# Optimization experiments

Measured on AMD Instinct MI355X. Metric: run time of the kernel, lower is better.

Reference implementation:

```python
import jax, jax.numpy as jnp
import numpy as np
import math

D = 1280      # embed_dim ('650M')
H = 20        # n_head
DH = D // H   # d_hidden = 64
DFF = 4 * D   # r_ff = 4
LN_EPS = 1e-5


def layer_norm(x, gamma, beta):
    mu = jnp.mean(x, axis=-1, keepdims=True)
    var = jnp.var(x, axis=-1, keepdims=True)
    return (x - mu) * jax.lax.rsqrt(var + LN_EPS) * gamma + beta


def setup_inputs() -> dict:
    key = jax.random.key(0)
    ks = jax.random.split(key, 16)
    B, L = 2, 2048
    x = jax.random.normal(ks[0], (B, L, D), dtype=jnp.float32)
    y = jax.random.normal(ks[1], (B, L, D), dtype=jnp.float32)  # dm_embeds (unused by module)
    s_qkv = 1.0 / math.sqrt(D)
    Wq = jax.random.uniform(ks[2], (D, D), jnp.float32, -s_qkv, s_qkv)
    Wk = jax.random.uniform(ks[3], (D, D), jnp.float32, -s_qkv, s_qkv)
    Wv = jax.random.uniform(ks[4], (D, D), jnp.float32, -s_qkv, s_qkv)
    Wo = jax.random.uniform(ks[5], (D, D), jnp.float32, -s_qkv, s_qkv)
    bo = jnp.zeros((D,), jnp.float32)
    W1 = jax.random.normal(ks[6], (D, DFF), jnp.float32) * math.sqrt(2.0 / D)  # kaiming
    b1 = jnp.zeros((DFF,), jnp.float32)
    W2 = jax.random.uniform(ks[7], (DFF, D), jnp.float32, -1.0 / math.sqrt(DFF), 1.0 / math.sqrt(DFF))
    b2 = jnp.zeros((D,), jnp.float32)
    g1 = jnp.ones((D,), jnp.float32); be1 = jnp.zeros((D,), jnp.float32)
    g2 = jnp.ones((D,), jnp.float32); be2 = jnp.zeros((D,), jnp.float32)
    return dict(x=x, y=y, Wq=Wq, Wk=Wk, Wv=Wv, Wo=Wo, bo=bo,
                W1=W1, b1=b1, W2=W2, b2=b2, g1=g1, be1=be1, g2=g2, be2=be2)


def reference(x, y, Wq, Wk, Wv, Wo, bo, W1, b1, W2, b2, g1, be1, g2, be2):
    B, L, _ = x.shape
    scaling = 1.0 / math.sqrt(DH)
    # --- pre-norm self-attention ---
    xn = layer_norm(x, g1, be1)
    q = (xn @ Wq).reshape(B, L, H, DH) * scaling
    k = (xn @ Wk).reshape(B, L, H, DH)
    v = (xn @ Wv).reshape(B, L, H, DH)
    scores = jnp.einsum('bqhd,bkhd->bhqk', q, k)
    attn = jax.nn.softmax(scores, axis=-1)
    o = jnp.einsum('bhqk,bkhd->bqhd', attn, v).reshape(B, L, D)
    x = x + (o @ Wo + bo)
    # --- pre-norm FFN ---
    xn = layer_norm(x, g2, be2)
    h = jax.nn.relu(xn @ W1 + b1)
    x = x + (h @ W2 + b2)
    return x
```

## Files before the change

kernel.cpp:

```cpp
#include <hip/hip_runtime.h>

typedef short bf16x8 __attribute__((ext_vector_type(8)));
typedef short bf16x4 __attribute__((ext_vector_type(4)));
typedef float f32x4 __attribute__((ext_vector_type(4)));
typedef unsigned short u16;

#define GL16(g, l) __builtin_amdgcn_global_load_lds( \
    (const __attribute__((address_space(1))) void*)(g), \
    (__attribute__((address_space(3))) void*)(l), 16, 0, 0)

__device__ __forceinline__ u16 f2bf(float f) {
  union { float f; unsigned u; } v; v.f = f;
  return (u16)((v.u + 0x7fffu + ((v.u >> 16) & 1u)) >> 16);
}

__device__ __forceinline__ float exp2_(float x) {
#if __has_builtin(__builtin_amdgcn_exp2f)
  return __builtin_amdgcn_exp2f(x);
#else
  return __expf(x * 0.69314718056f);
#endif
}

__device__ __forceinline__ unsigned cvtpk(float a, float b) {
  unsigned r;
  asm("v_cvt_pk_bf16_f32 %0, %1, %2" : "=v"(r) : "v"(a), "v"(b));
  return r;
}

__global__ __launch_bounds__(256) void ln_kernel(
    const float* __restrict__ x, const float* __restrict__ g,
    const float* __restrict__ b, u16* __restrict__ out) {
  const int row = blockIdx.x, tid = threadIdx.x;
  const float4* xr = (const float4*)(x + (size_t)row * 1280);
  float4 v1 = xr[tid];
  float4 v2 = make_float4(0.f, 0.f, 0.f, 0.f);
  if (tid < 64) v2 = xr[256 + tid];
  float s = v1.x + v1.y + v1.z + v1.w + v2.x + v2.y + v2.z + v2.w;
  float q = v1.x * v1.x + v1.y * v1.y + v1.z * v1.z + v1.w * v1.w +
            v2.x * v2.x + v2.y * v2.y + v2.z * v2.z + v2.w * v2.w;
#pragma unroll
  for (int off = 32; off >= 1; off >>= 1) {
    s += __shfl_xor(s, off);
    q += __shfl_xor(q, off);
  }
  __shared__ float sm[8];
  if ((tid & 63) == 0) { sm[tid >> 6] = s; sm[4 + (tid >> 6)] = q; }
  __syncthreads();
  s = sm[0] + sm[1] + sm[2] + sm[3];
  q = sm[4] + sm[5] + sm[6] + sm[7];
  const float mean = s * (1.0f / 1280.0f);
  const float rstd = rsqrtf(q * (1.0f / 1280.0f) - mean * mean + 1e-5f);
  const float4* gr = (const float4*)g;
  const float4* br = (const float4*)b;
  u16* orow = out + (size_t)row * 1280;
  {
    float4 gg = gr[tid], bb = br[tid];
    ushort4 o;
    o.x = f2bf((v1.x - mean) * rstd * gg.x + bb.x);
    o.y = f2bf((v1.y - mean) * rstd * gg.y + bb.y);
    o.z = f2bf((v1.z - mean) * rstd * gg.z + bb.z);
    o.w = f2bf((v1.w - mean) * rstd * gg.w + bb.w);
    *(ushort4*)&orow[tid * 4] = o;
  }
  if (tid < 64) {
    float4 gg = gr[256 + tid], bb = br[256 + tid];
    ushort4 o;
    o.x = f2bf((v2.x - mean) * rstd * gg.x + bb.x);
    o.y = f2bf((v2.y - mean) * rstd * gg.y + bb.y);
    o.z = f2bf((v2.z - mean) * rstd * gg.z + bb.z);
    o.w = f2bf((v2.w - mean) * rstd * gg.w + bb.w);
    *(ushort4*)&orow[(256 + tid) * 4] = o;
  }
}

__global__ __launch_bounds__(256) void tconv_kernel(
    const float* __restrict__ src, u16* __restrict__ dst,
    int rows, int cols, float scale) {
  __shared__ float t[64][33];
  const int tid = threadIdx.x;
  const size_t c0 = (size_t)blockIdx.x * 64, r0 = (size_t)blockIdx.y * 32;
  const int ty = tid >> 4, col4 = tid & 15;
#pragma unroll
  for (int i = 0; i < 2; ++i) {
    const int row = ty + i * 16;
    float4 v = *(const float4*)&src[(r0 + row) * cols + c0 + col4 * 4];
    t[col4 * 4 + 0][row] = v.x;
    t[col4 * 4 + 1][row] = v.y;
    t[col4 * 4 + 2][row] = v.z;
    t[col4 * 4 + 3][row] = v.w;
  }
  __syncthreads();
  const int c = tid >> 2, rb = (tid & 3) * 8;
  ushort4 o1, o2;
  o1.x = f2bf(t[c][rb + 0] * scale); o1.y = f2bf(t[c][rb + 1] * scale);
  o1.z = f2bf(t[c][rb + 2] * scale); o1.w = f2bf(t[c][rb + 3] * scale);
  o2.x = f2bf(t[c][rb + 4] * scale); o2.y = f2bf(t[c][rb + 5] * scale);
  o2.z = f2bf(t[c][rb + 6] * scale); o2.w = f2bf(t[c][rb + 7] * scale);
  u16* d = &dst[(c0 + c) * rows + r0 + rb];
  *(ushort4*)d = o1;
  *(ushort4*)(d + 4) = o2;
}

__global__ __launch_bounds__(256) void tconv3_kernel(
    const float* __restrict__ s0, const float* __restrict__ s1,
    const float* __restrict__ s2, u16* __restrict__ dst, float scale0) {
  __shared__ float t[64][33];
  const int tid = threadIdx.x, z = blockIdx.z;
  const float* src = (z == 0) ? s0 : ((z == 1) ? s1 : s2);
  const float scale = (z == 0) ? scale0 : 1.0f;
  u16* d0 = dst + (size_t)z * 1280 * 1280;
  const size_t c0 = (size_t)blockIdx.x * 64, r0 = (size_t)blockIdx.y * 32;
  const int ty = tid >> 4, col4 = tid & 15;
#pragma unroll
  for (int i = 0; i < 2; ++i) {
    const int row = ty + i * 16;
    float4 v = *(const float4*)&src[(r0 + row) * 1280 + c0 + col4 * 4];
    t[col4 * 4 + 0][row] = v.x;
    t[col4 * 4 + 1][row] = v.y;
    t[col4 * 4 + 2][row] = v.z;
    t[col4 * 4 + 3][row] = v.w;
  }
  __syncthreads();
  const int c = tid >> 2, rb = (tid & 3) * 8;
  ushort4 o1, o2;
  o1.x = f2bf(t[c][rb + 0] * scale); o1.y = f2bf(t[c][rb + 1] * scale);
  o1.z = f2bf(t[c][rb + 2] * scale); o1.w = f2bf(t[c][rb + 3] * scale);
  o2.x = f2bf(t[c][rb + 4] * scale); o2.y = f2bf(t[c][rb + 5] * scale);
  o2.z = f2bf(t[c][rb + 6] * scale); o2.w = f2bf(t[c][rb + 7] * scale);
  u16* d = &d0[(c0 + c) * 1280 + r0 + rb];
  *(ushort4*)d = o1;
  *(ushort4*)(d + 4) = o2;
}

__global__ __launch_bounds__(256) void vtrans_kernel(const u16* __restrict__ qkv,
                                                     u16* __restrict__ vt) {
  __shared__ u16 t[64][65];
  const int tx = threadIdx.x & 63, ty = threadIdx.x >> 6;
  const int t0 = blockIdx.x * 64, bh = blockIdx.y, b = bh / 20, h = bh % 20;
  const u16* src = qkv + (size_t)b * 2048 * 3840 + 2560 + h * 64;
  for (int i = ty; i < 64; i += 4) t[i][tx] = src[(size_t)(t0 + i) * 3840 + tx];
  __syncthreads();
  u16* dst = vt + (size_t)bh * 64 * 2048 + t0;
  for (int i = ty; i < 64; i += 4) dst[(size_t)i * 2048 + tx] = t[tx][i];
}

__global__ __launch_bounds__(256) void initadd_kernel(
    const float* __restrict__ src, const float* __restrict__ bias,
    float* __restrict__ out) {
  const size_t i = (size_t)blockIdx.x * 256 + threadIdx.x;
  float4 v = ((const float4*)src)[i];
  float4 b = ((const float4*)bias)[i % 320];
  v.x += b.x; v.y += b.y; v.z += b.z; v.w += b.w;
  ((float4*)out)[i] = v;
}

template <int EPI>
__device__ __forceinline__ void gemm_body(
    const u16* __restrict__ A, const u16* __restrict__ BT,
    const float* __restrict__ bias, void* __restrict__ out,
    int M, int N, int K, int kSteps) {
  __shared__ __attribute__((aligned(16))) u16 Als[3][128 * 32];
  __shared__ __attribute__((aligned(16))) u16 Bls[3][128 * 32];
  const int tid = threadIdx.x;
  const int w = tid >> 6, lane = tid & 63;
  const int lo = lane & 15, hi = lane >> 4;
  const int wm = w >> 1, wn = w & 1;
  const int gx = gridDim.x, gxy = gx * gridDim.y;
  const int nwg = gxy * gridDim.z;
  int s = blockIdx.x + gx * blockIdx.y + gxy * blockIdx.z;
  s = (s & 7) * (nwg >> 3) + (s >> 3);
  const int bz = s / gxy; s -= bz * gxy;
  const int by = s / gx;  const int bx = s - by * gx;
  const size_t m0 = (size_t)by * 128, n0 = (size_t)bx * 128;
  const int kt0 = bz * kSteps;
  f32x4 acc[4][4] = {};
  const int srow = w * 32 + (lane >> 2);
  const int scol = ((lane & 3) ^ ((lane >> 3) & 3)) * 8;
  const int rsw = (lo >> 1) & 3;
#define STAGE(buf, kt)                                                        \
  do {                                                                        \
    const size_t kb = (size_t)(kt) * 32 + scol;                               \
    GL16(&A[(m0 + srow) * K + kb],       &Als[buf][(w * 2 + 0) * 512]);       \
    GL16(&A[(m0 + srow + 16) * K + kb],  &Als[buf][(w * 2 + 1) * 512]);       \
    GL16(&BT[(n0 + srow) * K + kb],      &Bls[buf][(w * 2 + 0) * 512]);       \
    GL16(&BT[(n0 + srow + 16) * K + kb], &Bls[buf][(w * 2 + 1) * 512]);       \
  } while (0)
  STAGE(0, kt0 + 0);
  STAGE(1, kt0 + 1);
  int cur = 0;
  for (int t = 0; t < kSteps; ++t) {
    if (t + 1 < kSteps) asm volatile("s_waitcnt vmcnt(4)" ::: "memory");
    else                asm volatile("s_waitcnt vmcnt(0)" ::: "memory");
    __builtin_amdgcn_s_barrier();
    __builtin_amdgcn_sched_barrier(0);
    const int nxt = (cur == 0) ? 2 : cur - 1;
    if (t + 2 < kSteps) STAGE(nxt, kt0 + t + 2);
    bf16x8 af[4], bfr[4];
#pragma unroll
    for (int mi = 0; mi < 4; ++mi)
      af[mi] = *(const bf16x8*)&Als[cur][(wm * 64 + mi * 16 + lo) * 32 + ((hi ^ rsw) * 8)];
#pragma unroll
    for (int ni = 0; ni < 4; ++ni)
      bfr[ni] = *(const bf16x8*)&Bls[cur][(wn * 64 + ni * 16 + lo) * 32 + ((hi ^ rsw) * 8)];
#pragma unroll
    for (int mi = 0; mi < 4; ++mi)
#pragma unroll
      for (int ni = 0; ni < 4; ++ni)
        acc[mi][ni] = __builtin_amdgcn_mfma_f32_16x16x32_bf16(
            af[mi], bfr[ni], acc[mi][ni], 0, 0, 0);
    cur = (cur == 2) ? 0 : cur + 1;
  }
#undef STAGE
#pragma unroll
  for (int ni = 0; ni < 4; ++ni) {
    const size_t col = n0 + wn * 64 + ni * 16 + lo;
    const float bv = (EPI == 1) ? bias[col] : 0.0f;
#pragma unroll
    for (int mi = 0; mi < 4; ++mi) {
      const size_t rb = m0 + wm * 64 + mi * 16 + hi * 4;
#pragma unroll
      for (int r = 0; r < 4; ++r) {
        const size_t idx = (rb + r) * N + col;
        float v = acc[mi][ni][r];
        if (EPI == 0) {
          ((u16*)out)[idx] = f2bf(v);
        } else if (EPI == 1) {
          v += bv;
          v = fmaxf(v, 0.0f);
          ((u16*)out)[idx] = f2bf(v);
        } else {
          atomicAdd(&((float*)out)[idx], v);
        }
      }
    }
  }
}

__global__ __launch_bounds__(256, 3) void gemm_qkv(
    const u16* __restrict__ A, const u16* __restrict__ BT,
    void* __restrict__ out, int M, int N, int K, int kSteps) {
  gemm_body<0>(A, BT, nullptr, out, M, N, K, kSteps);
}
__global__ __launch_bounds__(256, 3) void gemm_oproj(
    const u16* __restrict__ A, const u16* __restrict__ BT,
    void* __restrict__ out, int M, int N, int K, int kSteps) {
  gemm_body<3>(A, BT, nullptr, out, M, N, K, kSteps);
}
__global__ __launch_bounds__(256, 3) void gemm_ffn1(
    const u16* __restrict__ A, const u16* __restrict__ BT,
    const float* __restrict__ bias, void* __restrict__ out,
    int M, int N, int K, int kSteps) {
  gemm_body<1>(A, BT, bias, out, M, N, K, kSteps);
}
__global__ __launch_bounds__(256, 3) void gemm_ffn2(
    const u16* __restrict__ A, const u16* __restrict__ BT,
    void* __restrict__ out, int M, int N, int K, int kSteps) {
  gemm_body<3>(A, BT, nullptr, out, M, N, K, kSteps);
}

__global__ __launch_bounds__(256) void attn_kernel(
    const u16* __restrict__ qkv, const u16* __restrict__ vt,
    u16* __restrict__ aout) {
  __shared__ __attribute__((aligned(16))) u16 Klds[64 * 64];
  __shared__ __attribute__((aligned(16))) u16 Vlds[64 * 64];
  __shared__ __attribute__((aligned(16))) u16 Plds[4][16][72];
  const int tid = threadIdx.x;
  const int w = tid >> 6, lane = tid & 63;
  const int lo = lane & 15, hi = lane >> 4;
  const int bh = blockIdx.x, qt = blockIdx.y;
  const int b = bh / 20, h = bh % 20;
  const size_t qrow = (size_t)b * 2048 + qt * 64 + w * 16 + lo;
  bf16x8 qf[2];
  qf[0] = *(const bf16x8*)&qkv[qrow * 3840 + h * 64 + hi * 8];
  qf[1] = *(const bf16x8*)&qkv[qrow * 3840 + h * 64 + 32 + hi * 8];
  float m_i = -1e30f, l_i = 0.0f;
  f32x4 accO[4] = {};
  const int srow = lane >> 3;
  const int scol = ((lane & 7) ^ srow) * 8;
  const u16* kbase = qkv + (size_t)b * 2048 * 3840 + 1280 + h * 64;
  const u16* vbase = vt + (size_t)bh * 64 * 2048;
  for (int kt = 0; kt < 32; ++kt) {
#pragma unroll
    for (int c = 0; c < 2; ++c) {
      const int chunk = w * 2 + c;
      const int row = chunk * 8 + srow;
      GL16(kbase + (size_t)(kt * 64 + row) * 3840 + scol, &Klds[chunk * 512]);
      GL16(vbase + (size_t)row * 2048 + kt * 64 + scol, &Vlds[chunk * 512]);
    }
    __syncthreads();
    f32x4 s4[4] = {};
    __builtin_amdgcn_s_setprio(1);
#pragma unroll
    for (int st = 0; st < 4; ++st) {
      const int row = st * 16 + lo;
      const int sw = (row & 7) << 3;
#pragma unroll
      for (int ks = 0; ks < 2; ++ks) {
        bf16x8 a = *(const bf16x8*)&Klds[row * 64 + ((ks * 32 + hi * 8) ^ sw)];
        s4[st] = __builtin_amdgcn_mfma_f32_16x16x32_bf16(a, qf[ks], s4[st], 0, 0, 0);
      }
    }
    __builtin_amdgcn_s_setprio(0);
    float tm = fmaxf(fmaxf(fmaxf(s4[0][0], s4[0][1]), fmaxf(s4[0][2], s4[0][3])),
                     fmaxf(fmaxf(s4[1][0], s4[1][1]), fmaxf(s4[1][2], s4[1][3])));
    tm = fmaxf(tm, fmaxf(fmaxf(fmaxf(s4[2][0], s4[2][1]), fmaxf(s4[2][2], s4[2][3])),
                         fmaxf(fmaxf(s4[3][0], s4[3][1]), fmaxf(s4[3][2], s4[3][3]))));
    tm = fmaxf(tm, __shfl_xor(tm, 16));
    tm = fmaxf(tm, __shfl_xor(tm, 32));
    if (!__all(tm <= m_i + 8.0f)) {
      const float mnew = fmaxf(m_i, tm);
      const float corr = exp2_(m_i - mnew);
      m_i = mnew;
      l_i *= corr;
      float cr[4];
#pragma unroll
      for (int r = 0; r < 4; ++r) cr[r] = __shfl(corr, hi * 4 + r);
#pragma unroll
      for (int d = 0; d < 4; ++d)
#pragma unroll
        for (int r = 0; r < 4; ++r) accO[d][r] *= cr[r];
    }
#pragma unroll
    for (int st = 0; st < 4; ++st)
#pragma unroll
      for (int r = 0; r < 4; ++r) {
        const float p = exp2_(s4[st][r] - m_i);
        s4[st][r] = p;
        l_i += p;
      }
#pragma unroll
    for (int st = 0; st < 4; ++st) {
      uint2 pk;
      pk.x = cvtpk(s4[st][0], s4[st][1]);
      pk.y = cvtpk(s4[st][2], s4[st][3]);
      *(uint2*)&Plds[w][lo][st * 16 + hi * 4] = pk;
    }
    asm volatile("s_waitcnt lgkmcnt(0)" ::: "memory");
    __builtin_amdgcn_sched_barrier(0);
    __builtin_amdgcn_s_setprio(1);
#pragma unroll
    for (int ks = 0; ks < 2; ++ks) {
      bf16x8 pa = *(const bf16x8*)&Plds[w][lo][ks * 32 + hi * 8];
#pragma unroll
      for (int d = 0; d < 4; ++d) {
        const int row = d * 16 + lo;
        bf16x8 vb = *(const bf16x8*)
            &Vlds[row * 64 + ((ks * 32 + hi * 8) ^ ((row & 7) << 3))];
        accO[d] = __builtin_amdgcn_mfma_f32_16x16x32_bf16(pa, vb, accO[d], 0, 0, 0);
      }
    }
    __builtin_amdgcn_s_setprio(0);
    __syncthreads();
  }
  l_i += __shfl_xor(l_i, 16);
  l_i += __shfl_xor(l_i, 32);
  float linv[4];
#pragma unroll
  for (int r = 0; r < 4; ++r) linv[r] = 1.0f / __shfl(l_i, hi * 4 + r);
  const size_t orow0 = (size_t)b * 2048 + qt * 64 + w * 16 + hi * 4;
#pragma unroll
  for (int d = 0; d < 4; ++d)
#pragma unroll
    for (int r = 0; r < 4; ++r)
      aout[(orow0 + r) * 1280 + h * 64 + d * 16 + lo] =
          f2bf(accO[d][r] * linv[r]);
}

extern "C" void kernel_launch(void* const* d_in, const int* in_sizes, int n_in,
                              void* d_out, int out_size, void* d_ws, size_t ws_size,
                              hipStream_t stream) {
  const float* x   = (const float*)d_in[0];
  const float* Wq  = (const float*)d_in[2];
  const float* Wk  = (const float*)d_in[3];
  const float* Wv  = (const float*)d_in[4];
  const float* Wo  = (const float*)d_in[5];
  const float* bo  = (const float*)d_in[6];
  const float* W1  = (const float*)d_in[7];
  const float* b1  = (const float*)d_in[8];
  const float* W2  = (const float*)d_in[9];
  const float* b2  = (const float*)d_in[10];
  const float* g1  = (const float*)d_in[11];
  const float* be1 = (const float*)d_in[12];
  const float* g2  = (const float*)d_in[13];
  const float* be2 = (const float*)d_in[14];

  u16* xn   = (u16*)d_ws;
  u16* Wqkv = xn + (size_t)4096 * 1280;
  u16* WoT  = Wqkv + (size_t)3840 * 1280;
  u16* W1T  = WoT + (size_t)1280 * 1280;
  u16* W2T  = W1T + (size_t)5120 * 1280;
  u16* aOut = W2T + (size_t)1280 * 5120;
  float* x1 = (float*)(aOut + (size_t)4096 * 1280);
  u16* qkvb = (u16*)(x1 + (size_t)4096 * 1280);
  u16* vtb  = qkvb + (size_t)4096 * 3840;
  u16* hbuf = qkvb;

  const float qscale = 0.125f * 1.4426950408889634f;
  ln_kernel<<<4096, 256, 0, stream>>>(x, g1, be1, xn);
  tconv3_kernel<<<dim3(20, 40, 3), 256, 0, stream>>>(Wq, Wk, Wv, Wqkv, qscale);
  tconv_kernel<<<dim3(20, 40), 256, 0, stream>>>(Wo, WoT, 1280, 1280, 1.0f);
  tconv_kernel<<<dim3(80, 40), 256, 0, stream>>>(W1, W1T, 1280, 5120, 1.0f);
  tconv_kernel<<<dim3(20, 160), 256, 0, stream>>>(W2, W2T, 5120, 1280, 1.0f);
  gemm_qkv<<<dim3(30, 32), 256, 0, stream>>>(xn, Wqkv, qkvb, 4096, 3840, 1280, 40);
  vtrans_kernel<<<dim3(32, 40), 256, 0, stream>>>(qkvb, vtb);
  attn_kernel<<<dim3(40, 32), 256, 0, stream>>>(qkvb, vtb, aOut);
  initadd_kernel<<<5120, 256, 0, stream>>>(x, bo, x1);
  gemm_oproj<<<dim3(10, 32, 2), 256, 0, stream>>>(aOut, WoT, x1, 4096, 1280, 1280, 20);
  ln_kernel<<<4096, 256, 0, stream>>>(x1, g2, be2, xn);
  gemm_ffn1<<<dim3(40, 32), 256, 0, stream>>>(xn, W1T, b1, hbuf, 4096, 5120, 1280, 40);
  initadd_kernel<<<5120, 256, 0, stream>>>(x1, b2, (float*)d_out);
  gemm_ffn2<<<dim3(10, 32, 2), 256, 0, stream>>>(hbuf, W2T, d_out, 4096, 1280, 5120, 80);
  (void)in_sizes; (void)n_in; (void)out_size; (void)ws_size;
}
```

Measured before the change: 411.3 us.

## Switch GEMMs to 256x256 tiles with an 8-wave, four-phase ping-pong schedule

Replaces the 128x128, 4-wave, triple-buffered GEMM body with a 256x256 tile computed by 8 waves and a K-step of 64. Each K-step is split into four barrier-separated quadrants that interleave LDS fragment reads, global-to-LDS prefetch of the next A/B halves, and MFMA bursts raised with s_setprio. The aim is more reuse per byte loaded and better overlap of loads with matrix math. In exchange the grids become much smaller (for example 240 or 320 blocks), split-K factors change, and the roughly 128 KB of LDS per block allows only one block per CU. That makes wave quantization and tail effects a real risk.

```diff
diff --git a/kernel.cpp b/kernel.cpp
--- a/kernel.cpp
+++ b/kernel.cpp
@@ -156,69 +156,151 @@
 }
 
 template <int EPI>
-__device__ __forceinline__ void gemm_body(
+__device__ __forceinline__ void gemm8_body(
     const u16* __restrict__ A, const u16* __restrict__ BT,
     const float* __restrict__ bias, void* __restrict__ out,
-    int M, int N, int K, int kSteps) {
-  __shared__ __attribute__((aligned(16))) u16 Als[3][128 * 32];
-  __shared__ __attribute__((aligned(16))) u16 Bls[3][128 * 32];
+    int M, int N, int K, int nt) {
+  __shared__ __attribute__((aligned(16))) u16 Als[2][256 * 64];
+  __shared__ __attribute__((aligned(16))) u16 Bls[2][256 * 64];
   const int tid = threadIdx.x;
   const int w = tid >> 6, lane = tid & 63;
   const int lo = lane & 15, hi = lane >> 4;
-  const int wm = w >> 1, wn = w & 1;
+  const int wm = w >> 2, wn = w & 3;
   const int gx = gridDim.x, gxy = gx * gridDim.y;
   const int nwg = gxy * gridDim.z;
   int s = blockIdx.x + gx * blockIdx.y + gxy * blockIdx.z;
   s = (s & 7) * (nwg >> 3) + (s >> 3);
   const int bz = s / gxy; s -= bz * gxy;
   const int by = s / gx;  const int bx = s - by * gx;
-  const size_t m0 = (size_t)by * 128, n0 = (size_t)bx * 128;
-  const int kt0 = bz * kSteps;
-  f32x4 acc[4][4] = {};
-  const int srow = w * 32 + (lane >> 2);
-  const int scol = ((lane & 3) ^ ((lane >> 3) & 3)) * 8;
-  const int rsw = (lo >> 1) & 3;
-#define STAGE(buf, kt)                                                        \
+  const size_t m0 = (size_t)by * 256, n0 = (size_t)bx * 256;
+  const int kt0 = bz * nt;
+  f32x4 acc[8][4] = {};
+  const int srowo = lane >> 3;
+  const int gcol = ((lane & 7) ^ (lane >> 3)) * 8;
+  const int rsw = lo & 7;
+#define STG_A(buf, kt, half)                                                  \
   do {                                                                        \
-    const size_t kb = (size_t)(kt) * 32 + scol;                               \
-    GL16(&A[(m0 + srow) * K + kb],       &Als[buf][(w * 2 + 0) * 512]);       \
-    GL16(&A[(m0 + srow + 16) * K + kb],  &Als[buf][(w * 2 + 1) * 512]);       \
-    GL16(&BT[(n0 + srow) * K + kb],      &Bls[buf][(w * 2 + 0) * 512]);       \
-    GL16(&BT[(n0 + srow + 16) * K + kb], &Bls[buf][(w * 2 + 1) * 512]);       \
+    const int rc = (half) * 128 + w * 16;                                     \
+    const size_t kb = (size_t)(kt) * 64 + gcol;                               \
+    GL16(&A[(m0 + rc + srowo) * K + kb],     &Als[buf][rc * 64]);             \
+    GL16(&A[(m0 + rc + 8 + srowo) * K + kb], &Als[buf][(rc + 8) * 64]);       \
   } while (0)
-  STAGE(0, kt0 + 0);
-  STAGE(1, kt0 + 1);
-  int cur = 0;
-  for (int t = 0; t < kSteps; ++t) {
-    if (t + 1 < kSteps) asm volatile("s_waitcnt vmcnt(4)" ::: "memory");
-    else                asm volatile("s_waitcnt vmcnt(0)" ::: "memory");
-    __builtin_amdgcn_s_barrier();
-    __builtin_amdgcn_sched_barrier(0);
-    const int nxt = (cur == 0) ? 2 : cur - 1;
-    if (t + 2 < kSteps) STAGE(nxt, kt0 + t + 2);
-    bf16x8 af[4], bfr[4];
-#pragma unroll
-    for (int mi = 0; mi < 4; ++mi)
-      af[mi] = *(const bf16x8*)&Als[cur][(wm * 64 + mi * 16 + lo) * 32 + ((hi ^ rsw) * 8)];
-#pragma unroll
-    for (int ni = 0; ni < 4; ++ni)
-      bfr[ni] = *(const bf16x8*)&Bls[cur][(wn * 64 + ni * 16 + lo) * 32 + ((hi ^ rsw) * 8)];
-#pragma unroll
-    for (int mi = 0; mi < 4; ++mi)
-#pragma unroll
-      for (int ni = 0; ni < 4; ++ni)
-        acc[mi][ni] = __builtin_amdgcn_mfma_f32_16x16x32_bf16(
-            af[mi], bfr[ni], acc[mi][ni], 0, 0, 0);
-    cur = (cur == 2) ? 0 : cur + 1;
-  }
-#undef STAGE
+#define STG_B(buf, kt, half)                                                  \
+  do {                                                                        \
+    const int rc = (half) * 128 + w * 16;                                     \
+    const size_t kb = (size_t)(kt) * 64 + gcol;                               \
+    GL16(&BT[(n0 + rc + srowo) * K + kb],     &Bls[buf][rc * 64]);            \
+    GL16(&BT[(n0 + rc + 8 + srowo) * K + kb], &Bls[buf][(rc + 8) * 64]);      \
+  } while (0)
+#define BAR()  __builtin_amdgcn_s_barrier()
+#define SB0()  __builtin_amdgcn_sched_barrier(0)
+#define LGKM0() asm volatile("s_waitcnt lgkmcnt(0)" ::: "memory")
+  STG_A(0, kt0 + 0, 0); STG_A(0, kt0 + 0, 1);
+  STG_B(0, kt0 + 0, 0); STG_B(0, kt0 + 0, 1);
+  STG_B(1, kt0 + 1, 0); STG_B(1, kt0 + 1, 1);
+  SB0();
+  asm volatile("s_waitcnt vmcnt(4)" ::: "memory");
+  BAR(); SB0();
+  for (int t = 0; t < nt; ++t) {
+    const int c = t & 1;
+    const u16* Ac = Als[c];
+    const u16* Bc = Bls[c];
+    bf16x8 a0[4][2], a1[4][2], b0[2][2], b1[2][2];
+#pragma unroll
+    for (int mi = 0; mi < 4; ++mi)
+#pragma unroll
+      for (int ks = 0; ks < 2; ++ks)
+        a0[mi][ks] = *(const bf16x8*)&Ac[(wm * 128 + mi * 16 + lo) * 64 +
+                                        (((ks * 4 + hi) ^ rsw) * 8)];
+#pragma unroll
+    for (int ni = 0; ni < 2; ++ni)
+#pragma unroll
+      for (int ks = 0; ks < 2; ++ks)
+        b0[ni][ks] = *(const bf16x8*)&Bc[(wn * 64 + ni * 16 + lo) * 64 +
+                                        (((ks * 4 + hi) ^ rsw) * 8)];
+    if (t + 1 < nt) STG_A(c ^ 1, kt0 + t + 1, 0);
+    BAR(); LGKM0(); SB0();
+    __builtin_amdgcn_s_setprio(1);
+#pragma unroll
+    for (int mi = 0; mi < 4; ++mi)
+#pragma unroll
+      for (int ni = 0; ni < 2; ++ni)
+#pragma unroll
+        for (int ks = 0; ks < 2; ++ks)
+          acc[mi][ni] = __builtin_amdgcn_mfma_f32_16x16x32_bf16(
+              a0[mi][ks], b0[ni][ks], acc[mi][ni], 0, 0, 0);
+    __builtin_amdgcn_s_setprio(0);
+    BAR(); SB0();
+#pragma unroll
+    for (int ni = 0; ni < 2; ++ni)
+#pragma unroll
+      for (int ks = 0; ks < 2; ++ks)
+        b1[ni][ks] = *(const bf16x8*)&Bc[(wn * 64 + (ni + 2) * 16 + lo) * 64 +
+                                        (((ks * 4 + hi) ^ rsw) * 8)];
+    if (t + 1 < nt) STG_A(c ^ 1, kt0 + t + 1, 1);
+    BAR(); LGKM0(); SB0();
+    __builtin_amdgcn_s_setprio(1);
+#pragma unroll
+    for (int mi = 0; mi < 4; ++mi)
+#pragma unroll
+      for (int ni = 0; ni < 2; ++ni)
+#pragma unroll
+        for (int ks = 0; ks < 2; ++ks)
+          acc[mi][ni + 2] = __builtin_amdgcn_mfma_f32_16x16x32_bf16(
+              a0[mi][ks], b1[ni][ks], acc[mi][ni + 2], 0, 0, 0);
+    __builtin_amdgcn_s_setprio(0);
+    BAR(); SB0();
+#pragma unroll
+    for (int mi = 0; mi < 4; ++mi)
+#pragma unroll
+      for (int ks = 0; ks < 2; ++ks)
+        a1[mi][ks] = *(const bf16x8*)&Ac[(wm * 128 + (mi + 4) * 16 + lo) * 64 +
+                                        (((ks * 4 + hi) ^ rsw) * 8)];
+    if (t + 2 < nt) STG_B(c, kt0 + t + 2, 0);
+    BAR(); LGKM0(); SB0();
+    __builtin_amdgcn_s_setprio(1);
+#pragma unroll
+    for (int mi = 0; mi < 4; ++mi)
+#pragma unroll
+      for (int ni = 0; ni < 2; ++ni)
+#pragma unroll
+        for (int ks = 0; ks < 2; ++ks)
+          acc[mi + 4][ni] = __builtin_amdgcn_mfma_f32_16x16x32_bf16(
+              a1[mi][ks], b0[ni][ks], acc[mi + 4][ni], 0, 0, 0);
+    __builtin_amdgcn_s_setprio(0);
+    BAR(); SB0();
+    if (t + 2 < nt) {
+      STG_B(c, kt0 + t + 2, 1);
+      SB0();
+      asm volatile("s_waitcnt vmcnt(4)" ::: "memory");
+    } else {
+      asm volatile("s_waitcnt vmcnt(0)" ::: "memory");
+    }
+    BAR(); SB0();
+    __builtin_amdgcn_s_setprio(1);
+#pragma unroll
+    for (int mi = 0; mi < 4; ++mi)
+#pragma unroll
+      for (int ni = 0; ni < 2; ++ni)
+#pragma unroll
+        for (int ks = 0; ks < 2; ++ks)
+          acc[mi + 4][ni + 2] = __builtin_amdgcn_mfma_f32_16x16x32_bf16(
+              a1[mi][ks], b1[ni][ks], acc[mi + 4][ni + 2], 0, 0, 0);
+    __builtin_amdgcn_s_setprio(0);
+    BAR(); SB0();
+  }
+#undef STG_A
+#undef STG_B
+#undef BAR
+#undef SB0
+#undef LGKM0
 #pragma unroll
   for (int ni = 0; ni < 4; ++ni) {
     const size_t col = n0 + wn * 64 + ni * 16 + lo;
     const float bv = (EPI == 1) ? bias[col] : 0.0f;
 #pragma unroll
-    for (int mi = 0; mi < 4; ++mi) {
-      const size_t rb = m0 + wm * 64 + mi * 16 + hi * 4;
+    for (int mi = 0; mi < 8; ++mi) {
+      const size_t rb = m0 + wm * 128 + mi * 16 + hi * 4;
 #pragma unroll
       for (int r = 0; r < 4; ++r) {
         const size_t idx = (rb + r) * N + col;
@@ -237,26 +319,26 @@
   }
 }
 
-__global__ __launch_bounds__(256, 3) void gemm_qkv(
+__global__ __launch_bounds__(512, 2) void gemm_qkv(
     const u16* __restrict__ A, const u16* __restrict__ BT,
-    void* __restrict__ out, int M, int N, int K, int kSteps) {
-  gemm_body<0>(A, BT, nullptr, out, M, N, K, kSteps);
-}
-__global__ __launch_bounds__(256, 3) void gemm_oproj(
+    void* __restrict__ out, int M, int N, int K, int nt) {
+  gemm8_body<0>(A, BT, nullptr, out, M, N, K, nt);
+}
+__global__ __launch_bounds__(512, 2) void gemm_oproj(
     const u16* __restrict__ A, const u16* __restrict__ BT,
-    void* __restrict__ out, int M, int N, int K, int kSteps) {
-  gemm_body<3>(A, BT, nullptr, out, M, N, K, kSteps);
-}
-__global__ __launch_bounds__(256, 3) void gemm_ffn1(
+    void* __restrict__ out, int M, int N, int K, int nt) {
+  gemm8_body<3>(A, BT, nullptr, out, M, N, K, nt);
+}
+__global__ __launch_bounds__(512, 2) void gemm_ffn1(
     const u16* __restrict__ A, const u16* __restrict__ BT,
     const float* __restrict__ bias, void* __restrict__ out,
-    int M, int N, int K, int kSteps) {
-  gemm_body<1>(A, BT, bias, out, M, N, K, kSteps);
-}
-__global__ __launch_bounds__(256, 3) void gemm_ffn2(
+    int M, int N, int K, int nt) {
+  gemm8_body<1>(A, BT, bias, out, M, N, K, nt);
+}
+__global__ __launch_bounds__(512, 2) void gemm_ffn2(
     const u16* __restrict__ A, const u16* __restrict__ BT,
-    void* __restrict__ out, int M, int N, int K, int kSteps) {
-  gemm_body<3>(A, BT, nullptr, out, M, N, K, kSteps);
+    void* __restrict__ out, int M, int N, int K, int nt) {
+  gemm8_body<3>(A, BT, nullptr, out, M, N, K, nt);
 }
 
 __global__ __launch_bounds__(256) void attn_kernel(
@@ -402,14 +484,14 @@
   tconv_kernel<<<dim3(20, 40), 256, 0, stream>>>(Wo, WoT, 1280, 1280, 1.0f);
   tconv_kernel<<<dim3(80, 40), 256, 0, stream>>>(W1, W1T, 1280, 5120, 1.0f);
   tconv_kernel<<<dim3(20, 160), 256, 0, stream>>>(W2, W2T, 5120, 1280, 1.0f);
-  gemm_qkv<<<dim3(30, 32), 256, 0, stream>>>(xn, Wqkv, qkvb, 4096, 3840, 1280, 40);
+  gemm_qkv<<<dim3(15, 16), 512, 0, stream>>>(xn, Wqkv, qkvb, 4096, 3840, 1280, 20);
   vtrans_kernel<<<dim3(32, 40), 256, 0, stream>>>(qkvb, vtb);
   attn_kernel<<<dim3(40, 32), 256, 0, stream>>>(qkvb, vtb, aOut);
   initadd_kernel<<<5120, 256, 0, stream>>>(x, bo, x1);
-  gemm_oproj<<<dim3(10, 32, 2), 256, 0, stream>>>(aOut, WoT, x1, 4096, 1280, 1280, 20);
+  gemm_oproj<<<dim3(5, 16, 2), 512, 0, stream>>>(aOut, WoT, x1, 4096, 1280, 1280, 10);
   ln_kernel<<<4096, 256, 0, stream>>>(x1, g2, be2, xn);
-  gemm_ffn1<<<dim3(40, 32), 256, 0, stream>>>(xn, W1T, b1, hbuf, 4096, 5120, 1280, 40);
+  gemm_ffn1<<<dim3(20, 16), 512, 0, stream>>>(xn, W1T, b1, hbuf, 4096, 5120, 1280, 20);
   initadd_kernel<<<5120, 256, 0, stream>>>(x1, b2, (float*)d_out);
-  gemm_ffn2<<<dim3(10, 32, 2), 256, 0, stream>>>(hbuf, W2T, d_out, 4096, 1280, 5120, 80);
+  gemm_ffn2<<<dim3(5, 16, 4), 512, 0, stream>>>(hbuf, W2T, d_out, 4096, 1280, 5120, 20);
   (void)in_sizes; (void)n_in; (void)out_size; (void)ws_size;
 }
```

Measured after the change: 442.6 us. 7.6% more time.
